# Kernel tuning notes

Measured on AMD Instinct MI355X. Metric: run time of the kernel, lower is better.

Reference implementation:

```python
import jax, jax.numpy as jnp
import numpy as np

B, N, D, NH, L, DFF = 2, 2048, 256, 8, 4, 1024
DH = D // NH
FACTOR = 0.5 / float(np.sqrt(DH))  # == 1/sqrt(4*DH), matches q/k feature dim 4*d_head
EPS = 1e-5


def _ln(x, g, b):
    m = x.mean(-1, keepdims=True)
    v = ((x - m) ** 2).mean(-1, keepdims=True)
    return (x - m) * jax.lax.rsqrt(v + EPS) * g + b


def setup_inputs() -> dict:
    key = jax.random.key(0)
    ks = jax.random.split(key, 16)
    s = 0.05
    r = lambda i, shape: jax.random.normal(ks[i], shape, dtype=jnp.float32)
    return {
        "H": r(0, (B, N, D)),
        "V": r(1, (B, N, 3, D)),
        "D_batch": r(2, (B, N, N)),
        "rbf_feat": r(3, (L, B, 1, N, N)),
        "H_mask": jnp.ones((B, N), dtype=bool),
        "ln1_g": jnp.ones((L, D)), "ln1_b": jnp.zeros((L, D)),
        "ln2_g": jnp.ones((L, D)), "ln2_b": jnp.zeros((L, D)),
        "Wq": r(4, (L, D, 4 * D)) * s, "bq": jnp.zeros((L, 4 * D)),
        "Wk": r(5, (L, D, 4 * D)) * s, "bk": jnp.zeros((L, 4 * D)),
        "Wv": r(6, (L, D, D)) * s, "bv": jnp.zeros((L, D)),
        "Wvv": r(7, (L, D, D)) * s,
        "Wo": r(8, (L, D, D)) * s, "bo": jnp.zeros((L, D)),
        "Wvo": r(9, (L, D, D)) * s,
        "Wlv": r(10, (L, D, 2 * D)) * s,
        "W1": r(11, (L, 2 * D, DFF)) * s, "b1": jnp.zeros((L, DFF)),
        "W2": r(12, (L, DFF, 2 * D)) * s, "b2": jnp.zeros((L, 2 * D)),
    }


def _stack_forward(H, V, D_batch, rbf_feat, H_mask, ln1_g, ln1_b, ln2_g, ln2_b,
                   Wq, bq, Wk, bk, Wv, bv, Wvv, Wo, bo, Wvo, Wlv, W1, b1, W2, b2):
    b, n = H.shape[:2]
    mask = H_mask[:, None, None, :]       # [B,1,1,N] masks key columns
    base_bias = D_batch[:, None]          # [B,1,N,N]

    def step(carry, xs):
        H, V = carry
        (rbf, g1, be1, g2, be2, wq, bq_, wk, bk_, wv, bv_, wvv,
         wo, bo_, wvo, wlv, w1, b1_, w2, b2_) = xs
        # --- self-attention sublayer (pre-LN on scalar stream only) ---
        Hn = _ln(H, g1, be1)
        Hq = (Hn @ wq + bq_).reshape(b, n, NH, 4 * DH)
        Hk = (Hn @ wk + bk_).reshape(b, n, NH, 4 * DH)
        Hv = (Hn @ wv + bv_).reshape(b, n, NH, DH)
        Vv = (V @ wvv).reshape(b, n, 3, NH, DH)
        Vv = jnp.swapaxes(Vv, 2, 3).reshape(b, n, NH, 3 * DH)
        V_attn = jnp.concatenate([Hv, Vv], axis=-1)        # [B,N,H,4*DH]
        bias = jnp.where(mask, rbf + base_bias, -jnp.inf)  # [B,1,N,N]
        scores = jnp.einsum('bnhd,bmhd->bhnm', Hq, Hk) * FACTOR + bias
        attn = jax.nn.softmax(scores, axis=-1)
        res = jnp.einsum('bhnm,bmhd->bnhd', attn, V_attn)  # [B,N,H,4*DH]
        H_res = res[..., :DH].reshape(b, n, D)
        V_res = jnp.swapaxes(res[..., DH:].reshape(b, n, NH, 3, DH), 2, 3).reshape(b, n, 3, D)
        H = H + (H_res @ wo + bo_)
        V = V + V_res @ wvo
        # --- GVP FFN sublayer (pre-LN on scalar stream only) ---
        Hn = _ln(H, g2, be2)
        Vp = V @ wlv                                       # [B,N,3,2D]
        V1, V2 = Vp[..., :D], Vp[..., D:]
        scaler = jnp.concatenate([Hn, jnp.linalg.norm(V1, axis=-2)], axis=-1)
        sc = jax.nn.silu(scaler @ w1 + b1_) @ w2 + b2_
        H = H + sc[..., :D]
        V = V + sc[..., D:][..., None, :] * V2             # vector_act='none'
        return (H, V), None

    xs = (rbf_feat, ln1_g, ln1_b, ln2_g, ln2_b, Wq, bq, Wk, bk, Wv, bv, Wvv,
          Wo, bo, Wvo, Wlv, W1, b1, W2, b2)
    (H, V), _ = jax.lax.scan(step, (H, V), xs)
    return H, V


def reference(H, V, D_batch, rbf_feat, H_mask, ln1_g, ln1_b, ln2_g, ln2_b,
              Wq, bq, Wk, bk, Wv, bv, Wvv, Wo, bo, Wvo, Wlv, W1, b1, W2, b2):
    return _stack_forward(H, V, D_batch, rbf_feat, H_mask, ln1_g, ln1_b, ln2_g, ln2_b,
                          Wq, bq, Wk, bk, Wv, bv, Wvv, Wo, bo, Wvo, Wlv, W1, b1, W2, b2)
```

## Files before the change

### kernel.cpp

```cpp
#include <hip/hip_runtime.h>
#include <math.h>

static constexpr int B_  = 2;
static constexpr int N_  = 2048;
static constexpr int D_  = 256;
static constexpr int NH_ = 8;
static constexpr int L_  = 4;
static constexpr int DH_ = 32;
static constexpr int DQ_ = 128;
static constexpr float FACTOR_ = 0.08838834764831845f;
static constexpr float EPS_ = 1e-5f;

typedef short    short8   __attribute__((ext_vector_type(8)));
typedef unsigned short us4 __attribute__((ext_vector_type(4)));
typedef unsigned short us8 __attribute__((ext_vector_type(8)));
typedef float    f32x4    __attribute__((ext_vector_type(4)));
typedef unsigned short us;

__device__ __forceinline__ us f2b(float f) {
  unsigned u = __float_as_uint(f);
  unsigned r = u + 0x7FFF + ((u >> 16) & 1);
  return (us)(r >> 16);
}
__device__ __forceinline__ float b2f(us u) {
  return __uint_as_float(((unsigned)u) << 16);
}
__device__ __forceinline__ void gl_lds16(const void* g, void* l) {
  __builtin_amdgcn_global_load_lds(
      (const __attribute__((address_space(1))) void*)g,
      (__attribute__((address_space(3))) void*)l, 16, 0, 0);
}

__global__ __launch_bounds__(256) void ln_kernel(const float* __restrict__ X,
    const float* __restrict__ g, const float* __restrict__ b,
    us* __restrict__ Y) {
  __shared__ float r1[256], r2[256];
  int row = blockIdx.x, tid = threadIdx.x;
  float x = X[(size_t)row * D_ + tid];
  r1[tid] = x; r2[tid] = x * x;
  __syncthreads();
  for (int s = 128; s > 0; s >>= 1) {
    if (tid < s) { r1[tid] += r1[tid + s]; r2[tid] += r2[tid + s]; }
    __syncthreads();
  }
  float mean = r1[0] * (1.0f / D_);
  float var  = r2[0] * (1.0f / D_) - mean * mean;
  float inv  = rsqrtf(var + EPS_);
  Y[(size_t)row * D_ + tid] = f2b((x - mean) * inv * g[tid] + b[tid]);
}

__global__ __launch_bounds__(256) void conv_bf16(const float* __restrict__ X,
    us* __restrict__ Y) {
  size_t i = ((size_t)blockIdx.x * 256 + threadIdx.x) * 4;
  float4 v = *(const float4*)&X[i];
  us4 o = { f2b(v.x), f2b(v.y), f2b(v.z), f2b(v.w) };
  *(us4*)&Y[i] = o;
}

struct WConvDesc {
  const float* src[9];
  unsigned dst[9];
  int K[9];
  int N[9];
  int start[10];
};
__global__ __launch_bounds__(256) void wconv_kernel(WConvDesc d, us* __restrict__ Wb) {
  __shared__ float T[64][65];
  int bid = blockIdx.x, tid = threadIdx.x;
  int j = 0;
  #pragma unroll
  for (int q = 0; q < 8; q++) if (bid >= d.start[q + 1]) j = q + 1;
  int t = bid - d.start[j];
  int K = d.K[j], N = d.N[j];
  int tpr = N >> 6;
  int tk = t / tpr, tn = t - tk * tpr;
  const float* src = d.src[j];
  us* dst = Wb + d.dst[j];
  #pragma unroll
  for (int i = 0; i < 4; i++) {
    int r = i * 16 + (tid >> 4), c = (tid & 15) * 4;
    *(float4*)&T[r][c] = *(const float4*)&src[(size_t)(tk * 64 + r) * N + tn * 64 + c];
  }
  __syncthreads();
  #pragma unroll
  for (int i = 0; i < 4; i++) {
    int n = i * 16 + (tid >> 4), k = (tid & 15) * 4;
    us4 o = { f2b(T[k][n]), f2b(T[k + 1][n]), f2b(T[k + 2][n]), f2b(T[k + 3][n]) };
    *(us4*)&dst[(size_t)(tn * 64 + n) * K + tk * 64 + k] = o;
  }
}

template<int BIG, int BIAS, int ACC, int SILU, int WF, int WB, int QK>
__global__ __launch_bounds__(256, 2) void gemm_v2(const us* __restrict__ A,
    const us* __restrict__ Wt, const float* __restrict__ bias,
    const float* __restrict__ bias2, float* __restrict__ Cf, us* __restrict__ Cb,
    int M, int K, int Nc, float oscale) {
  constexpr int BM  = BIG ? 128 : 64;
  constexpr int NF  = BIG ? 4 : 2;
  constexpr int WS  = NF * 16;
  constexpr int NLD = BM / 32;
  __shared__ us As[2][BM * 64];
  __shared__ us Bs[2][BM * 64];
  const int tid = threadIdx.x;
  const int w = tid >> 6, l = tid & 63;
  const int lx = l & 15, ly = l >> 4;
  const int wr = w >> 1, wc = w & 1;
  const int bn = blockIdx.x, bm = blockIdx.y;
  const int swz = (lx & 7) << 4;
  const char* Ag = (const char*)A + (size_t)(bm * BM) * K * 2;
  const char* Bg = (const char*)Wt + (size_t)(bn * BM) * K * 2;
  const size_t rowb = (size_t)K * 2;

  #define GSTAGE(buf, k0)                                                     \
    do {                                                                      \
      _Pragma("unroll")                                                       \
      for (int j = 0; j < NLD; j++) {                                         \
        int o = j * 4096 + tid * 16;                                          \
        int r = o >> 7, cb = o & 127;                                         \
        int sc = cb ^ ((r & 7) << 4);                                         \
        gl_lds16(Ag + (size_t)r * rowb + (size_t)(k0) * 2 + sc,               \
                 &As[buf][(j * 4096 + w * 1024) >> 1]);                       \
        gl_lds16(Bg + (size_t)r * rowb + (size_t)(k0) * 2 + sc,               \
                 &Bs[buf][(j * 4096 + w * 1024) >> 1]);                       \
      }                                                                       \
    } while (0)

  f32x4 acc[NF][NF];
  #pragma unroll
  for (int i = 0; i < NF; i++)
    #pragma unroll
    for (int j = 0; j < NF; j++) acc[i][j] = (f32x4){0.f, 0.f, 0.f, 0.f};

  int cur = 0;
  GSTAGE(0, 0);
  __syncthreads();
  for (int k0 = 0; k0 < K; k0 += 64) {
    if (k0 + 64 < K) GSTAGE(cur ^ 1, k0 + 64);
    #pragma unroll
    for (int s = 0; s < 2; s++) {
      short8 af[NF], bf[NF];
      #pragma unroll
      for (int mt = 0; mt < NF; mt++)
        af[mt] = *(const short8*)
            &As[cur][(((wr * WS + mt * 16 + lx) * 128) + ((s * 64 + ly * 16) ^ swz)) >> 1];
      #pragma unroll
      for (int nt = 0; nt < NF; nt++)
        bf[nt] = *(const short8*)
            &Bs[cur][(((wc * WS + nt * 16 + lx) * 128) + ((s * 64 + ly * 16) ^ swz)) >> 1];
      __builtin_amdgcn_s_setprio(1);
      #pragma unroll
      for (int mt = 0; mt < NF; mt++)
        #pragma unroll
        for (int nt = 0; nt < NF; nt++)
          acc[mt][nt] = __builtin_amdgcn_mfma_f32_16x16x32_bf16(af[mt], bf[nt], acc[mt][nt], 0, 0, 0);
      __builtin_amdgcn_s_setprio(0);
    }
    __syncthreads();
    cur ^= 1;
  }
  #undef GSTAGE

  #pragma unroll
  for (int nt = 0; nt < NF; nt++) {
    const int n = bn * BM + wc * WS + nt * 16 + lx;
    float bval = 0.f, osc = oscale;
    if (QK) {
      bval = (n < 1024) ? bias[n] : bias2[n - 1024];
      osc = (n < 1024) ? oscale : 1.0f;
    } else if (BIAS) {
      bval = bias[n];
    }
    #pragma unroll
    for (int mt = 0; mt < NF; mt++) {
      #pragma unroll
      for (int r = 0; r < 4; r++) {
        const int m = bm * BM + wr * WS + mt * 16 + ly * 4 + r;
        float v = acc[mt][nt][r] + bval;
        if (SILU) v = v / (1.f + __expf(-v));
        size_t idx = (size_t)m * Nc + n;
        if (ACC) v += Cf[idx];
        if (WF) Cf[idx] = v;
        if (WB) Cb[idx] = f2b(v * osc);
      }
    }
  }
}

__global__ __launch_bounds__(256) void pack_vattn_t(const us* __restrict__ Hv,
    const us* __restrict__ Vv, us* __restrict__ Vt) {
  __shared__ us T[64][136];
  const int bid = blockIdx.x;
  const int nt = bid & 31, hh = (bid >> 5) & 7, b = bid >> 8;
  const int n0 = nt * 64;
  const int tid = threadIdx.x;
  {
    const int nn = tid >> 2, part = tid & 3;
    const size_t row = (size_t)(b * N_ + n0 + nn);
    const us* src = (part == 0) ? (Hv + row * D_ + hh * DH_)
                                : (Vv + (row * 3 + (part - 1)) * D_ + hh * DH_);
    #pragma unroll
    for (int jj = 0; jj < 32; jj += 8)
      *(us8*)&T[nn][part * 32 + jj] = *(const us8*)(src + jj);
  }
  __syncthreads();
  const int d = tid >> 1, half = tid & 1;
  size_t ob = ((size_t)(b * NH_ + hh) * DQ_ + d) * (size_t)N_ + n0 + half * 32;
  #pragma unroll
  for (int i = 0; i < 32; i += 8) {
    us8 o;
    #pragma unroll
    for (int e = 0; e < 8; e++) o[e] = T[half * 32 + i + e][d];
    *(us8*)&Vt[ob + i] = o;
  }
}

__global__ __launch_bounds__(256, 2) void attn_mfma(
    const us* __restrict__ QKb,
    const us* __restrict__ Vtb,
    const float* __restrict__ rbf,
    const float* __restrict__ Db,
    us* __restrict__ Hres,
    us* __restrict__ Vres) {
  __shared__ us Kt[2][8192];
  __shared__ us Vt[2][8192];
  __shared__ us Plds[4][16][72];
  const int bid = blockIdx.x;
  const int h  = bid >> 6;
  const int g  = bid & 63;
  const int b  = g >> 5;
  const int qt = g & 31;
  const int tid = threadIdx.x;
  const int w  = tid >> 6;
  const int l  = tid & 63;
  const int lx = l & 15;
  const int ly = l >> 4;
  const int qrow = qt * 64 + w * 16 + lx;
  const int swz = (lx & 7) << 4;

  short8 qf[4];
  {
    const us* qp = QKb + (size_t)(b * N_ + qrow) * 2048 + h * DQ_ + ly * 8;
    #pragma unroll
    for (int s = 0; s < 4; s++) qf[s] = *(const short8*)(qp + s * 32);
  }
  const char* kg = (const char*)QKb + (size_t)b * N_ * 4096 + 2048 + h * 256;
  const char* vg = (const char*)(Vtb + ((size_t)(b * NH_ + h) * DQ_) * (size_t)N_);
  const float* rbase = rbf + ((size_t)b * N_ + qrow) * N_;
  const float* dbase = Db  + ((size_t)b * N_ + qrow) * N_;

  #define STAGE(buf, m0)                                                      \
    do {                                                                      \
      _Pragma("unroll")                                                       \
      for (int j = 0; j < 4; j++) {                                           \
        int o = j * 4096 + tid * 16;                                          \
        int r = o >> 8, cb = o & 255;                                         \
        int scb = cb ^ ((r & 7) << 4);                                        \
        gl_lds16(kg + (size_t)((m0) + r) * 4096 + scb,                        \
                 &Kt[buf][(j * 4096 + w * 1024) >> 1]);                       \
      }                                                                       \
      _Pragma("unroll")                                                       \
      for (int j = 0; j < 4; j++) {                                           \
        int o = j * 4096 + tid * 16;                                          \
        int r = o >> 7, cb = o & 127;                                         \
        int scb = cb ^ ((r & 7) << 4);                                        \
        gl_lds16(vg + (size_t)r * (N_ * 2) + (size_t)(m0) * 2 + scb,          \
                 &Vt[buf][(j * 4096 + w * 1024) >> 1]);                       \
      }                                                                       \
    } while (0)

  float m_run = -3.0e38f, l_run = 0.f;
  f32x4 oacc[8];
  #pragma unroll
  for (int i = 0; i < 8; i++) oacc[i] = (f32x4){0.f, 0.f, 0.f, 0.f};

  int cur = 0;
  STAGE(0, 0);
  __syncthreads();

  for (int mc0 = 0; mc0 < N_; mc0 += 64) {
    if (mc0 + 64 < N_) STAGE(cur ^ 1, mc0 + 64);
    float4 r4[4], d4[4];
    #pragma unroll
    for (int t = 0; t < 4; t++) {
      r4[t] = *(const float4*)(rbase + mc0 + t * 16 + ly * 4);
      d4[t] = *(const float4*)(dbase + mc0 + t * 16 + ly * 4);
    }
    f32x4 sacc[4];
    #pragma unroll
    for (int t = 0; t < 4; t++) sacc[t] = (f32x4){0.f, 0.f, 0.f, 0.f};
    __builtin_amdgcn_s_setprio(1);
    #pragma unroll
    for (int t = 0; t < 4; t++) {
      #pragma unroll
      for (int s = 0; s < 4; s++) {
        const short8 kf = *(const short8*)
            &Kt[cur][((t * 16 + lx) * 256 + ((s * 64 + ly * 16) ^ swz)) >> 1];
        sacc[t] = __builtin_amdgcn_mfma_f32_16x16x32_bf16(kf, qf[s], sacc[t], 0, 0, 0);
      }
    }
    __builtin_amdgcn_s_setprio(0);
    float pvv[16];
    #pragma unroll
    for (int t = 0; t < 4; t++) {
      pvv[t*4+0] = sacc[t][0] + r4[t].x + d4[t].x;
      pvv[t*4+1] = sacc[t][1] + r4[t].y + d4[t].y;
      pvv[t*4+2] = sacc[t][2] + r4[t].z + d4[t].z;
      pvv[t*4+3] = sacc[t][3] + r4[t].w + d4[t].w;
    }
    float a8[8], a4[4];
    #pragma unroll
    for (int i = 0; i < 8; i++) a8[i] = fmaxf(pvv[i], pvv[i + 8]);
    #pragma unroll
    for (int i = 0; i < 4; i++) a4[i] = fmaxf(a8[i], a8[i + 4]);
    float mloc = fmaxf(fmaxf(a4[0], a4[1]), fmaxf(a4[2], a4[3]));
    mloc = fmaxf(mloc, __shfl_xor(mloc, 16, 64));
    mloc = fmaxf(mloc, __shfl_xor(mloc, 32, 64));
    if (!__all(mloc - m_run <= 8.0f)) {
      float m_new = fmaxf(m_run, mloc);
      float scale = __expf(m_run - m_new);
      l_run *= scale;
      #pragma unroll
      for (int i = 0; i < 8; i++) {
        oacc[i][0] *= scale; oacc[i][1] *= scale;
        oacc[i][2] *= scale; oacc[i][3] *= scale;
      }
      m_run = m_new;
    }
    float s8[8], s4[4];
    #pragma unroll
    for (int i = 0; i < 16; i++) pvv[i] = __expf(pvv[i] - m_run);
    #pragma unroll
    for (int i = 0; i < 8; i++) s8[i] = pvv[i] + pvv[i + 8];
    #pragma unroll
    for (int i = 0; i < 4; i++) s4[i] = s8[i] + s8[i + 4];
    float lloc = (s4[0] + s4[1]) + (s4[2] + s4[3]);
    lloc += __shfl_xor(lloc, 16, 64);
    lloc += __shfl_xor(lloc, 32, 64);
    l_run += lloc;
    #pragma unroll
    for (int t = 0; t < 4; t++) {
      us4 pk = { f2b(pvv[t*4+0]), f2b(pvv[t*4+1]), f2b(pvv[t*4+2]), f2b(pvv[t*4+3]) };
      *(us4*)&Plds[w][lx][t * 16 + ly * 4] = pk;
    }
    short8 pf0 = *(const short8*)&Plds[w][lx][ly * 8];
    short8 pf1 = *(const short8*)&Plds[w][lx][32 + ly * 8];
    __builtin_amdgcn_s_setprio(1);
    #pragma unroll
    for (int dt = 0; dt < 8; dt++) {
      const int rb = (dt * 16 + lx) * 128;
      const short8 vf0 = *(const short8*)&Vt[cur][(rb + ((ly * 16) ^ swz)) >> 1];
      const short8 vf1 = *(const short8*)&Vt[cur][(rb + ((64 + ly * 16) ^ swz)) >> 1];
      oacc[dt] = __builtin_amdgcn_mfma_f32_16x16x32_bf16(vf0, pf0, oacc[dt], 0, 0, 0);
      oacc[dt] = __builtin_amdgcn_mfma_f32_16x16x32_bf16(vf1, pf1, oacc[dt], 0, 0, 0);
    }
    __builtin_amdgcn_s_setprio(0);
    __syncthreads();
    cur ^= 1;
  }
  #undef STAGE
  float inv = 1.0f / l_run;
  const size_t row = (size_t)(b * N_ + qrow);
  #pragma unroll
  for (int dt = 0; dt < 8; dt++) {
    const int d0 = dt * 16 + ly * 4;
    us4 pk = { f2b(oacc[dt][0] * inv), f2b(oacc[dt][1] * inv),
               f2b(oacc[dt][2] * inv), f2b(oacc[dt][3] * inv) };
    if (d0 < 32) {
      *(us4*)&Hres[row * D_ + h * DH_ + d0] = pk;
    } else {
      const int c = (d0 - DH_) >> 5, dd = (d0 - DH_) & 31;
      *(us4*)&Vres[(row * 3 + c) * D_ + h * DH_ + dd] = pk;
    }
  }
}

__global__ __launch_bounds__(256) void ln2scaler(const float* __restrict__ H,
    const float* __restrict__ g, const float* __restrict__ b,
    const float* __restrict__ Vp, us* __restrict__ scal) {
  __shared__ float r1[256], r2[256];
  size_t row = blockIdx.x;
  int j = threadIdx.x;
  float x = H[row * D_ + j];
  r1[j] = x; r2[j] = x * x;
  __syncthreads();
  for (int s = 128; s > 0; s >>= 1) {
    if (j < s) { r1[j] += r1[j + s]; r2[j] += r2[j + s]; }
    __syncthreads();
  }
  float mean = r1[0] * (1.0f / D_);
  float var  = r2[0] * (1.0f / D_) - mean * mean;
  float inv  = rsqrtf(var + EPS_);
  scal[row * 512 + j] = f2b((x - mean) * inv * g[j] + b[j]);
  float a  = Vp[(row * 3 + 0) * 512 + j];
  float c1 = Vp[(row * 3 + 1) * 512 + j];
  float c2 = Vp[(row * 3 + 2) * 512 + j];
  scal[row * 512 + D_ + j] = f2b(sqrtf(a * a + c1 * c1 + c2 * c2));
}

__global__ __launch_bounds__(256) void final_ln(float* __restrict__ H,
    float* __restrict__ V, const float* __restrict__ sc,
    const float* __restrict__ Vp, us* __restrict__ Vb,
    const float* __restrict__ g, const float* __restrict__ b,
    us* __restrict__ Hnb) {
  __shared__ float r1[256], r2[256];
  size_t row = blockIdx.x;
  int j = threadIdx.x;
  float hnew = H[row * D_ + j] + sc[row * 512 + j];
  H[row * D_ + j] = hnew;
  float s = sc[row * 512 + D_ + j];
  #pragma unroll
  for (int c = 0; c < 3; c++) {
    size_t vi = (row * 3 + c) * D_ + j;
    float nv = V[vi] + s * Vp[(row * 3 + c) * 512 + D_ + j];
    V[vi] = nv;
    Vb[vi] = f2b(nv);
  }
  if (g) {
    r1[j] = hnew; r2[j] = hnew * hnew;
    __syncthreads();
    for (int st = 128; st > 0; st >>= 1) {
      if (j < st) { r1[j] += r1[j + st]; r2[j] += r2[j + st]; }
      __syncthreads();
    }
    float mean = r1[0] * (1.0f / D_);
    float var  = r2[0] * (1.0f / D_) - mean * mean;
    float inv  = rsqrtf(var + EPS_);
    Hnb[row * D_ + j] = f2b((hnew - mean) * inv * g[j] + b[j]);
  }
}

extern "C" void kernel_launch(void* const* d_in, const int* in_sizes, int n_in,
                              void* d_out, int out_size, void* d_ws, size_t ws_size,
                              hipStream_t stream) {
  const float* H_in = (const float*)d_in[0];
  const float* V_in = (const float*)d_in[1];
  const float* Db   = (const float*)d_in[2];
  const float* rbf  = (const float*)d_in[3];
  const float* ln1g = (const float*)d_in[5];
  const float* ln1b = (const float*)d_in[6];
  const float* ln2g = (const float*)d_in[7];
  const float* ln2b = (const float*)d_in[8];
  const float* Wq  = (const float*)d_in[9];
  const float* bq  = (const float*)d_in[10];
  const float* Wk  = (const float*)d_in[11];
  const float* bk  = (const float*)d_in[12];
  const float* Wv  = (const float*)d_in[13];
  const float* bv  = (const float*)d_in[14];
  const float* Wvv = (const float*)d_in[15];
  const float* Wo  = (const float*)d_in[16];
  const float* bo  = (const float*)d_in[17];
  const float* Wvo = (const float*)d_in[18];
  const float* Wlv = (const float*)d_in[19];
  const float* W1  = (const float*)d_in[20];
  const float* b1  = (const float*)d_in[21];
  const float* W2  = (const float*)d_in[22];
  const float* b2  = (const float*)d_in[23];

  const size_t HN = (size_t)B_ * N_ * D_;
  const size_t VN = HN * 3;
  float* Hs = (float*)d_out;
  float* Vs = (float*)d_out + HN;
  float* ws = (float*)d_ws;
  us*    Wb     = (us*)(ws + 4194304);
  us*    Vb     = (us*)(ws + 5177344);
  us*    Hnb    = (us*)(ws + 6750208);
  us*    QKb    = (us*)(ws + 7274496);
  us*    Vtb    = (us*)(ws + 11468800);
  us*    Hvb    = (us*)(ws + 13565952);
  us*    Vvb    = (us*)(ws + 14090240);
  us*    Hres_b = (us*)(ws + 6750208);
  us*    Vres_b = (us*)(ws + 13565952);
  float* Vp     = ws + 7274496;
  us*    scal_b = (us*)(ws + 13565952);
  us*    midb   = (us*)(ws + 15014528);
  float* scb    = ws;

  hipMemcpyAsync(Hs, H_in, HN * sizeof(float), hipMemcpyDeviceToDevice, stream);
  hipMemcpyAsync(Vs, V_in, VN * sizeof(float), hipMemcpyDeviceToDevice, stream);
  conv_bf16<<<3072, 256, 0, stream>>>(V_in, Vb);

  const int ROWS  = B_ * N_;
  static const int wKs[9] = {256,256,256,256,256,256,256,512,1024};
  static const int wNs[9] = {1024,1024,256,256,256,256,512,1024,512};
  static const unsigned wOff[9] = {0,262144,524288,589824,655360,720896,786432,917504,1441792};
  static const int wStart[10] = {0,64,128,144,160,176,192,224,352,480};

  for (int l = 0; l < L_; ++l) {
    WConvDesc dsc;
    const float* srcs[9] = {
      Wq  + (size_t)l * 256 * 1024, Wk  + (size_t)l * 256 * 1024,
      Wv  + (size_t)l * 256 * 256,  Wvv + (size_t)l * 256 * 256,
      Wo  + (size_t)l * 256 * 256,  Wvo + (size_t)l * 256 * 256,
      Wlv + (size_t)l * 256 * 512,  W1  + (size_t)l * 512 * 1024,
      W2  + (size_t)l * 1024 * 512 };
    for (int j = 0; j < 9; j++) {
      dsc.src[j] = srcs[j]; dsc.dst[j] = wOff[j];
      dsc.K[j] = wKs[j]; dsc.N[j] = wNs[j]; dsc.start[j] = wStart[j];
    }
    dsc.start[9] = wStart[9];
    wconv_kernel<<<480, 256, 0, stream>>>(dsc, Wb);
    if (l == 0)
      ln_kernel<<<ROWS, 256, 0, stream>>>(Hs, ln1g, ln1b, Hnb);

    gemm_v2<1,1,0,0,0,1,1><<<dim3(16, 32), 256, 0, stream>>>(
        Hnb, Wb + wOff[0], bq + l * 1024, bk + l * 1024, nullptr, QKb, 4096, 256, 2048, FACTOR_);
    gemm_v2<0,1,0,0,0,1,0><<<dim3(4, 64), 256, 0, stream>>>(
        Hnb, Wb + wOff[2], bv + l * 256, nullptr, nullptr, Hvb, 4096, 256, 256, 1.f);
    gemm_v2<0,0,0,0,0,1,0><<<dim3(4, 192), 256, 0, stream>>>(
        Vb, Wb + wOff[3], nullptr, nullptr, nullptr, Vvb, 12288, 256, 256, 1.f);
    pack_vattn_t<<<512, 256, 0, stream>>>(Hvb, Vvb, Vtb);
    attn_mfma<<<512, 256, 0, stream>>>(QKb, Vtb,
        rbf + (size_t)l * B_ * N_ * N_, Db, Hres_b, Vres_b);
    gemm_v2<0,1,1,0,1,0,0><<<dim3(4, 64), 256, 0, stream>>>(
        Hres_b, Wb + wOff[4], bo + l * 256, nullptr, Hs, nullptr, 4096, 256, 256, 1.f);
    gemm_v2<0,0,1,0,1,1,0><<<dim3(4, 192), 256, 0, stream>>>(
        Vres_b, Wb + wOff[5], nullptr, nullptr, Vs, Vb, 12288, 256, 256, 1.f);
    gemm_v2<0,0,0,0,1,0,0><<<dim3(8, 192), 256, 0, stream>>>(
        Vb, Wb + wOff[6], nullptr, nullptr, Vp, nullptr, 12288, 256, 512, 1.f);
    ln2scaler<<<ROWS, 256, 0, stream>>>(Hs, ln2g + l * D_, ln2b + l * D_, Vp, scal_b);
    gemm_v2<1,1,0,1,0,1,0><<<dim3(8, 32), 256, 0, stream>>>(
        scal_b, Wb + wOff[7], b1 + l * 1024, nullptr, nullptr, midb, 4096, 512, 1024, 1.f);
    gemm_v2<0,1,0,0,1,0,0><<<dim3(8, 64), 256, 0, stream>>>(
        midb, Wb + wOff[8], b2 + l * 512, nullptr, scb, nullptr, 4096, 1024, 512, 1.f);
    final_ln<<<ROWS, 256, 0, stream>>>(Hs, Vs, scb, Vp, Vb,
        (l < 3) ? (ln1g + (l + 1) * D_) : nullptr,
        (l < 3) ? (ln1b + (l + 1) * D_) : nullptr, Hnb);
  }
}
```

Baseline: 846.4 us.

## Fuse QKV projection, precombine bf16 attention bias, merge output GEMMs, use exp2

Adds a biascomb kernel that sums rbf and distance bias per layer, scales by log2(e) and stores the result as bf16. Attention then reads one bf16 bias stream, prefetched one tile ahead, instead of two fp32 streams, which cuts the attention kernel's dominant memory traffic. The Q/K/V projections become one wider GEMM with log2e folded into the Q scale, so softmax can use exp2. The Wo and Wvo output GEMMs are merged into a single launch. The extra biascomb pass still reads both fp32 inputs each layer, and the bf16 bias rounding lowers softmax precision.

```diff
diff --git a/kernel.cpp b/kernel.cpp
--- a/kernel.cpp
+++ b/kernel.cpp
@@ -9,6 +9,7 @@
 static constexpr int DH_ = 32;
 static constexpr int DQ_ = 128;
 static constexpr float FACTOR_ = 0.08838834764831845f;
+static constexpr float LOG2E_  = 1.4426950408889634f;
 static constexpr float EPS_ = 1e-5f;
 
 typedef short    short8   __attribute__((ext_vector_type(8)));
@@ -24,6 +25,9 @@
 }
 __device__ __forceinline__ float b2f(us u) {
   return __uint_as_float(((unsigned)u) << 16);
+}
+__device__ __forceinline__ float e2(float x) {
+  return __builtin_amdgcn_exp2f(x);
 }
 __device__ __forceinline__ void gl_lds16(const void* g, void* l) {
   __builtin_amdgcn_global_load_lds(
@@ -57,6 +61,20 @@
   *(us4*)&Y[i] = o;
 }
 
+__global__ __launch_bounds__(256) void biascomb(const float* __restrict__ R,
+    const float* __restrict__ Dq, us* __restrict__ Out) {
+  size_t i = ((size_t)blockIdx.x * 256 + threadIdx.x) * 8;
+  float4 r0 = *(const float4*)&R[i];
+  float4 r1 = *(const float4*)&R[i + 4];
+  float4 d0 = *(const float4*)&Dq[i];
+  float4 d1 = *(const float4*)&Dq[i + 4];
+  us8 o = { f2b((r0.x + d0.x) * LOG2E_), f2b((r0.y + d0.y) * LOG2E_),
+            f2b((r0.z + d0.z) * LOG2E_), f2b((r0.w + d0.w) * LOG2E_),
+            f2b((r1.x + d1.x) * LOG2E_), f2b((r1.y + d1.y) * LOG2E_),
+            f2b((r1.z + d1.z) * LOG2E_), f2b((r1.w + d1.w) * LOG2E_) };
+  *(us8*)&Out[i] = o;
+}
+
 struct WConvDesc {
   const float* src[9];
   unsigned dst[9];
@@ -90,10 +108,11 @@
   }
 }
 
-template<int BIG, int BIAS, int ACC, int SILU, int WF, int WB, int QK>
+template<int BIG, int BIAS, int ACC, int SILU, int WF, int WB, int QKV>
 __global__ __launch_bounds__(256, 2) void gemm_v2(const us* __restrict__ A,
     const us* __restrict__ Wt, const float* __restrict__ bias,
-    const float* __restrict__ bias2, float* __restrict__ Cf, us* __restrict__ Cb,
+    const float* __restrict__ bias2, const float* __restrict__ bias3,
+    float* __restrict__ Cf, us* __restrict__ Cb,
     int M, int K, int Nc, float oscale) {
   constexpr int BM  = BIG ? 128 : 64;
   constexpr int NF  = BIG ? 4 : 2;
@@ -164,9 +183,10 @@
   for (int nt = 0; nt < NF; nt++) {
     const int n = bn * BM + wc * WS + nt * 16 + lx;
     float bval = 0.f, osc = oscale;
-    if (QK) {
-      bval = (n < 1024) ? bias[n] : bias2[n - 1024];
-      osc = (n < 1024) ? oscale : 1.0f;
+    if (QKV) {
+      if (n < 1024)      { bval = bias[n]; }
+      else if (n < 2048) { bval = bias2[n - 1024]; osc = 1.0f; }
+      else               { bval = bias3[n - 2048]; osc = 1.0f; }
     } else if (BIAS) {
       bval = bias[n];
     }
@@ -186,7 +206,98 @@
   }
 }
 
-__global__ __launch_bounds__(256) void pack_vattn_t(const us* __restrict__ Hv,
+__global__ __launch_bounds__(256, 2) void gemm_wo(const us* __restrict__ Hres,
+    const us* __restrict__ Vres, const us* __restrict__ WtO,
+    const us* __restrict__ WtVO, const float* __restrict__ bo,
+    float* __restrict__ Hs, float* __restrict__ Vs, us* __restrict__ Vb) {
+  constexpr int K = 256, Nc = 256;
+  __shared__ us As[2][64 * 64];
+  __shared__ us Bs[2][64 * 64];
+  const int tid = threadIdx.x;
+  const int w = tid >> 6, l = tid & 63;
+  const int lx = l & 15, ly = l >> 4;
+  const int wr = w >> 1, wc = w & 1;
+  const int bn = blockIdx.x, bm = blockIdx.y;
+  const bool isH = bm < 64;
+  const int mb = isH ? bm : bm - 64;
+  const int swz = (lx & 7) << 4;
+  const char* Ag = (const char*)(isH ? Hres : Vres) + (size_t)(mb * 64) * K * 2;
+  const char* Bg = (const char*)(isH ? WtO : WtVO) + (size_t)(bn * 64) * K * 2;
+  const size_t rowb = (size_t)K * 2;
+
+  #define GSTAGE(buf, k0)                                                     \
+    do {                                                                      \
+      _Pragma("unroll")                                                       \
+      for (int j = 0; j < 2; j++) {                                           \
+        int o = j * 4096 + tid * 16;                                          \
+        int r = o >> 7, cb = o & 127;                                         \
+        int sc = cb ^ ((r & 7) << 4);                                         \
+        gl_lds16(Ag + (size_t)r * rowb + (size_t)(k0) * 2 + sc,               \
+                 &As[buf][(j * 4096 + w * 1024) >> 1]);                       \
+        gl_lds16(Bg + (size_t)r * rowb + (size_t)(k0) * 2 + sc,               \
+                 &Bs[buf][(j * 4096 + w * 1024) >> 1]);                       \
+      }                                                                       \
+    } while (0)
+
+  f32x4 acc[2][2];
+  #pragma unroll
+  for (int i = 0; i < 2; i++)
+    #pragma unroll
+    for (int j = 0; j < 2; j++) acc[i][j] = (f32x4){0.f, 0.f, 0.f, 0.f};
+
+  int cur = 0;
+  GSTAGE(0, 0);
+  __syncthreads();
+  for (int k0 = 0; k0 < K; k0 += 64) {
+    if (k0 + 64 < K) GSTAGE(cur ^ 1, k0 + 64);
+    #pragma unroll
+    for (int s = 0; s < 2; s++) {
+      short8 af[2], bf[2];
+      #pragma unroll
+      for (int mt = 0; mt < 2; mt++)
+        af[mt] = *(const short8*)
+            &As[cur][(((wr * 32 + mt * 16 + lx) * 128) + ((s * 64 + ly * 16) ^ swz)) >> 1];
+      #pragma unroll
+      for (int nt = 0; nt < 2; nt++)
+        bf[nt] = *(const short8*)
+            &Bs[cur][(((wc * 32 + nt * 16 + lx) * 128) + ((s * 64 + ly * 16) ^ swz)) >> 1];
+      __builtin_amdgcn_s_setprio(1);
+      #pragma unroll
+      for (int mt = 0; mt < 2; mt++)
+        #pragma unroll
+        for (int nt = 0; nt < 2; nt++)
+          acc[mt][nt] = __builtin_amdgcn_mfma_f32_16x16x32_bf16(af[mt], bf[nt], acc[mt][nt], 0, 0, 0);
+      __builtin_amdgcn_s_setprio(0);
+    }
+    __syncthreads();
+    cur ^= 1;
+  }
+  #undef GSTAGE
+
+  #pragma unroll
+  for (int nt = 0; nt < 2; nt++) {
+    const int n = bn * 64 + wc * 32 + nt * 16 + lx;
+    const float bval = isH ? bo[n] : 0.f;
+    #pragma unroll
+    for (int mt = 0; mt < 2; mt++) {
+      #pragma unroll
+      for (int r = 0; r < 4; r++) {
+        const int m = mb * 64 + wr * 32 + mt * 16 + ly * 4 + r;
+        size_t idx = (size_t)m * Nc + n;
+        float v = acc[mt][nt][r] + bval;
+        if (isH) {
+          Hs[idx] += v;
+        } else {
+          float nv = Vs[idx] + v;
+          Vs[idx] = nv;
+          Vb[idx] = f2b(nv);
+        }
+      }
+    }
+  }
+}
+
+__global__ __launch_bounds__(256) void pack_vattn_t(const us* __restrict__ QKVb,
     const us* __restrict__ Vv, us* __restrict__ Vt) {
   __shared__ us T[64][136];
   const int bid = blockIdx.x;
@@ -196,7 +307,7 @@
   {
     const int nn = tid >> 2, part = tid & 3;
     const size_t row = (size_t)(b * N_ + n0 + nn);
-    const us* src = (part == 0) ? (Hv + row * D_ + hh * DH_)
+    const us* src = (part == 0) ? (QKVb + row * 2304 + 2048 + hh * DH_)
                                 : (Vv + (row * 3 + (part - 1)) * D_ + hh * DH_);
     #pragma unroll
     for (int jj = 0; jj < 32; jj += 8)
@@ -215,10 +326,9 @@
 }
 
 __global__ __launch_bounds__(256, 2) void attn_mfma(
-    const us* __restrict__ QKb,
+    const us* __restrict__ QKVb,
     const us* __restrict__ Vtb,
-    const float* __restrict__ rbf,
-    const float* __restrict__ Db,
+    const us* __restrict__ bias,
     us* __restrict__ Hres,
     us* __restrict__ Vres) {
   __shared__ us Kt[2][8192];
@@ -239,14 +349,13 @@
 
   short8 qf[4];
   {
-    const us* qp = QKb + (size_t)(b * N_ + qrow) * 2048 + h * DQ_ + ly * 8;
+    const us* qp = QKVb + (size_t)(b * N_ + qrow) * 2304 + h * DQ_ + ly * 8;
     #pragma unroll
     for (int s = 0; s < 4; s++) qf[s] = *(const short8*)(qp + s * 32);
   }
-  const char* kg = (const char*)QKb + (size_t)b * N_ * 4096 + 2048 + h * 256;
+  const char* kg = (const char*)QKVb + (size_t)b * N_ * 4608 + 2048 + h * 256;
   const char* vg = (const char*)(Vtb + ((size_t)(b * NH_ + h) * DQ_) * (size_t)N_);
-  const float* rbase = rbf + ((size_t)b * N_ + qrow) * N_;
-  const float* dbase = Db  + ((size_t)b * N_ + qrow) * N_;
+  const us* bbase = bias + ((size_t)b * N_ + qrow) * N_;
 
   #define STAGE(buf, m0)                                                      \
     do {                                                                      \
@@ -255,7 +364,7 @@
         int o = j * 4096 + tid * 16;                                          \
         int r = o >> 8, cb = o & 255;                                         \
         int scb = cb ^ ((r & 7) << 4);                                        \
-        gl_lds16(kg + (size_t)((m0) + r) * 4096 + scb,                        \
+        gl_lds16(kg + (size_t)((m0) + r) * 4608 + scb,                        \
                  &Kt[buf][(j * 4096 + w * 1024) >> 1]);                       \
       }                                                                       \
       _Pragma("unroll")                                                       \
@@ -275,15 +384,18 @@
 
   int cur = 0;
   STAGE(0, 0);
+  us4 bb[4];
+  #pragma unroll
+  for (int t = 0; t < 4; t++) bb[t] = *(const us4*)(bbase + t * 16 + ly * 4);
   __syncthreads();
 
   for (int mc0 = 0; mc0 < N_; mc0 += 64) {
-    if (mc0 + 64 < N_) STAGE(cur ^ 1, mc0 + 64);
-    float4 r4[4], d4[4];
-    #pragma unroll
-    for (int t = 0; t < 4; t++) {
-      r4[t] = *(const float4*)(rbase + mc0 + t * 16 + ly * 4);
-      d4[t] = *(const float4*)(dbase + mc0 + t * 16 + ly * 4);
+    us4 bbn[4];
+    if (mc0 + 64 < N_) {
+      STAGE(cur ^ 1, mc0 + 64);
+      #pragma unroll
+      for (int t = 0; t < 4; t++)
+        bbn[t] = *(const us4*)(bbase + mc0 + 64 + t * 16 + ly * 4);
     }
     f32x4 sacc[4];
     #pragma unroll
@@ -302,10 +414,10 @@
     float pvv[16];
     #pragma unroll
     for (int t = 0; t < 4; t++) {
-      pvv[t*4+0] = sacc[t][0] + r4[t].x + d4[t].x;
-      pvv[t*4+1] = sacc[t][1] + r4[t].y + d4[t].y;
-      pvv[t*4+2] = sacc[t][2] + r4[t].z + d4[t].z;
-      pvv[t*4+3] = sacc[t][3] + r4[t].w + d4[t].w;
+      pvv[t*4+0] = sacc[t][0] + b2f(bb[t][0]);
+      pvv[t*4+1] = sacc[t][1] + b2f(bb[t][1]);
+      pvv[t*4+2] = sacc[t][2] + b2f(bb[t][2]);
+      pvv[t*4+3] = sacc[t][3] + b2f(bb[t][3]);
     }
     float a8[8], a4[4];
     #pragma unroll
@@ -315,9 +427,9 @@
     float mloc = fmaxf(fmaxf(a4[0], a4[1]), fmaxf(a4[2], a4[3]));
     mloc = fmaxf(mloc, __shfl_xor(mloc, 16, 64));
     mloc = fmaxf(mloc, __shfl_xor(mloc, 32, 64));
-    if (!__all(mloc - m_run <= 8.0f)) {
+    if (!__all(mloc - m_run <= 11.54f)) {
       float m_new = fmaxf(m_run, mloc);
-      float scale = __expf(m_run - m_new);
+      float scale = e2(m_run - m_new);
       l_run *= scale;
       #pragma unroll
       for (int i = 0; i < 8; i++) {
@@ -328,7 +440,7 @@
     }
     float s8[8], s4[4];
     #pragma unroll
-    for (int i = 0; i < 16; i++) pvv[i] = __expf(pvv[i] - m_run);
+    for (int i = 0; i < 16; i++) pvv[i] = e2(pvv[i] - m_run);
     #pragma unroll
     for (int i = 0; i < 8; i++) s8[i] = pvv[i] + pvv[i + 8];
     #pragma unroll
@@ -356,6 +468,10 @@
     __builtin_amdgcn_s_setprio(0);
     __syncthreads();
     cur ^= 1;
+    if (mc0 + 64 < N_) {
+      #pragma unroll
+      for (int t = 0; t < 4; t++) bb[t] = bbn[t];
+    }
   }
   #undef STAGE
   float inv = 1.0f / l_run;
@@ -461,19 +577,19 @@
   float* Hs = (float*)d_out;
   float* Vs = (float*)d_out + HN;
   float* ws = (float*)d_ws;
+  us*    bias_b = (us*)ws;
   us*    Wb     = (us*)(ws + 4194304);
   us*    Vb     = (us*)(ws + 5177344);
   us*    Hnb    = (us*)(ws + 6750208);
-  us*    QKb    = (us*)(ws + 7274496);
-  us*    Vtb    = (us*)(ws + 11468800);
-  us*    Hvb    = (us*)(ws + 13565952);
+  us*    QKVb   = (us*)(ws + 7274496);
+  us*    Vtb    = (us*)(ws + 11993088);
   us*    Vvb    = (us*)(ws + 14090240);
   us*    Hres_b = (us*)(ws + 6750208);
-  us*    Vres_b = (us*)(ws + 13565952);
+  us*    Vres_b = (us*)(ws + 14090240);
   float* Vp     = ws + 7274496;
   us*    scal_b = (us*)(ws + 13565952);
   us*    midb   = (us*)(ws + 15014528);
-  float* scb    = ws;
+  float* scb    = ws + 2097152;
 
   hipMemcpyAsync(Hs, H_in, HN * sizeof(float), hipMemcpyDeviceToDevice, stream);
   hipMemcpyAsync(Vs, V_in, VN * sizeof(float), hipMemcpyDeviceToDevice, stream);
@@ -499,29 +615,26 @@
     }
     dsc.start[9] = wStart[9];
     wconv_kernel<<<480, 256, 0, stream>>>(dsc, Wb);
+    biascomb<<<4096, 256, 0, stream>>>(rbf + (size_t)l * B_ * N_ * N_, Db, bias_b);
     if (l == 0)
       ln_kernel<<<ROWS, 256, 0, stream>>>(Hs, ln1g, ln1b, Hnb);
 
-    gemm_v2<1,1,0,0,0,1,1><<<dim3(16, 32), 256, 0, stream>>>(
-        Hnb, Wb + wOff[0], bq + l * 1024, bk + l * 1024, nullptr, QKb, 4096, 256, 2048, FACTOR_);
-    gemm_v2<0,1,0,0,0,1,0><<<dim3(4, 64), 256, 0, stream>>>(
-        Hnb, Wb + wOff[2], bv + l * 256, nullptr, nullptr, Hvb, 4096, 256, 256, 1.f);
+    gemm_v2<1,0,0,0,0,1,1><<<dim3(18, 32), 256, 0, stream>>>(
+        Hnb, Wb + wOff[0], bq + l * 1024, bk + l * 1024, bv + l * 256,
+        nullptr, QKVb, 4096, 256, 2304, FACTOR_ * LOG2E_);
     gemm_v2<0,0,0,0,0,1,0><<<dim3(4, 192), 256, 0, stream>>>(
-        Vb, Wb + wOff[3], nullptr, nullptr, nullptr, Vvb, 12288, 256, 256, 1.f);
-    pack_vattn_t<<<512, 256, 0, stream>>>(Hvb, Vvb, Vtb);
-    attn_mfma<<<512, 256, 0, stream>>>(QKb, Vtb,
-        rbf + (size_t)l * B_ * N_ * N_, Db, Hres_b, Vres_b);
-    gemm_v2<0,1,1,0,1,0,0><<<dim3(4, 64), 256, 0, stream>>>(
-        Hres_b, Wb + wOff[4], bo + l * 256, nullptr, Hs, nullptr, 4096, 256, 256, 1.f);
-    gemm_v2<0,0,1,0,1,1,0><<<dim3(4, 192), 256, 0, stream>>>(
-        Vres_b, Wb + wOff[5], nullptr, nullptr, Vs, Vb, 12288, 256, 256, 1.f);
+        Vb, Wb + wOff[3], nullptr, nullptr, nullptr, nullptr, Vvb, 12288, 256, 256, 1.f);
+    pack_vattn_t<<<512, 256, 0, stream>>>(QKVb, Vvb, Vtb);
+    attn_mfma<<<512, 256, 0, stream>>>(QKVb, Vtb, bias_b, Hres_b, Vres_b);
+    gemm_wo<<<dim3(4, 256), 256, 0, stream>>>(
+        Hres_b, Vres_b, Wb + wOff[4], Wb + wOff[5], bo + l * 256, Hs, Vs, Vb);
     gemm_v2<0,0,0,0,1,0,0><<<dim3(8, 192), 256, 0, stream>>>(
-        Vb, Wb + wOff[6], nullptr, nullptr, Vp, nullptr, 12288, 256, 512, 1.f);
+        Vb, Wb + wOff[6], nullptr, nullptr, nullptr, Vp, nullptr, 12288, 256, 512, 1.f);
     ln2scaler<<<ROWS, 256, 0, stream>>>(Hs, ln2g + l * D_, ln2b + l * D_, Vp, scal_b);
     gemm_v2<1,1,0,1,0,1,0><<<dim3(8, 32), 256, 0, stream>>>(
-        scal_b, Wb + wOff[7], b1 + l * 1024, nullptr, nullptr, midb, 4096, 512, 1024, 1.f);
+        scal_b, Wb + wOff[7], b1 + l * 1024, nullptr, nullptr, nullptr, midb, 4096, 512, 1024, 1.f);
     gemm_v2<0,1,0,0,1,0,0><<<dim3(8, 64), 256, 0, stream>>>(
-        midb, Wb + wOff[8], b2 + l * 512, nullptr, scb, nullptr, 4096, 1024, 512, 1.f);
+        midb, Wb + wOff[8], b2 + l * 512, nullptr, nullptr, scb, nullptr, 4096, 1024, 512, 1.f);
     final_ln<<<ROWS, 256, 0, stream>>>(Hs, Vs, scb, Vp, Vb,
         (l < 3) ? (ln1g + (l + 1) * D_) : nullptr,
         (l < 3) ? (ln1b + (l + 1) * D_) : nullptr, Hnb);
```

Result: faster. 802.8 us (-5.2%).
